# Kernel tuning notes

Hardware: AMD Instinct MI355X
Metric: run time of the kernel (lower is better)

The kernel has to match this reference:

```python
import jax, jax.numpy as jnp
import numpy as np

B, N, C, H, W = 32, 8, 256, 4, 4


def setup_inputs() -> dict:
    key = jax.random.key(0)
    k1, k2 = jax.random.split(key)
    pred = jax.random.normal(k1, (B, N, C, H, W), dtype=jnp.float32)
    gt = jax.random.normal(k2, (B, N, C, H, W), dtype=jnp.float32)
    return {"pred": pred, "gt": gt}


def reference(pred, gt):
    b, n, c, h, w = pred.shape
    M = b * n * h * w
    # (B,N,C,H,W) -> (B,N,H,W,C) -> (M, C)
    p = jnp.transpose(pred, (0, 1, 3, 4, 2)).reshape(M, c)
    # (B,N,C,H,W) -> (C,B,N,H,W) -> (C, M)
    g = jnp.transpose(gt, (2, 0, 1, 3, 4)).reshape(c, M)
    lossmat = p @ g  # (M, M) similarity matrix
    # CrossEntropy with target = arange(M): -mean(log_softmax diag)
    logp = jax.nn.log_softmax(lossmat, axis=1)
    loss = -jnp.mean(jnp.diagonal(logp))
    # accuracy (no grad in original)
    top1 = jnp.argmax(lossmat, axis=1)
    acc = jnp.mean((top1 == jnp.arange(M)).astype(jnp.float32)) * 100.0
    return (loss, acc)
```

## Files before the change

kernel.cpp:

```cpp
#include <hip/hip_runtime.h>
#include <cstdint>

typedef __bf16 bf16x8 __attribute__((ext_vector_type(8)));
typedef float floatx4 __attribute__((ext_vector_type(4)));


#define OFF_X     (0u)
#define OFF_Y     (2u*1024*1024)
#define OFF_PMAX  (4u*1024*1024)
#define OFF_PSUM  (5u*1024*1024)
#define OFF_DIAG  (6u*1024*1024)
#define OFF_LPART (OFF_DIAG + 16384u)
#define OFF_CPART (OFF_LPART + 256u)
#define OFF_CNT   (OFF_CPART + 256u)

#define AS1C(p) ((const __attribute__((address_space(1))) void*)(const void*)(p))
#define AS3(p)  ((__attribute__((address_space(3))) void*)(void*)(p))

__global__ __launch_bounds__(256) void transpose_stage(
    const float* __restrict__ pred, const float* __restrict__ gt,
    unsigned short* __restrict__ Xs, unsigned short* __restrict__ Ys,
    int* __restrict__ cnt) {
  int blk = blockIdx.x;
  const int t = threadIdx.x;
  if (blk == 0 && t < 33) cnt[t] = 0;
  const float* src;
  unsigned short* dst;
  int slab;
  if (blk < 256) { src = pred; dst = Xs; slab = blk; }
  else           { src = gt;   dst = Ys; slab = blk - 256; }
  const float* sb = src + slab * 4096;
  const int rb = slab >> 3, rowhi = slab & 7;
  #pragma unroll
  for (int half = 0; half < 2; ++half) {
    int c_ = half * 256 + t;
    int rowlo = c_ & 15;
    int quad  = (c_ >> 4) & 3;
    int kk    = (c_ >> 6) & 1;
    int s     = c_ >> 7;
    int k0 = s * 64 + kk * 32 + quad * 8;
    unsigned int packed[4];
    #pragma unroll
    for (int jj = 0; jj < 4; ++jj) {
      unsigned int lohi[2];
      #pragma unroll
      for (int e = 0; e < 2; ++e) {
        float f = sb[(k0 + jj * 2 + e) * 16 + rowlo];
        unsigned int u = __float_as_uint(f);
        lohi[e] = (u + 0x7FFFu + ((u >> 16) & 1u)) >> 16;
      }
      packed[jj] = lohi[0] | (lohi[1] << 16);
    }
    unsigned short* o = dst + rb * 32768 +
        (unsigned)(s * 1024 + kk * 512 + rowhi * 64 + quad * 16 + rowlo) * 8;
    uint4 v; v.x = packed[0]; v.y = packed[1]; v.z = packed[2]; v.w = packed[3];
    *reinterpret_cast<uint4*>(o) = v;
  }
}

__global__ __launch_bounds__(512) void gemm_softmax_partial(
    const unsigned short* __restrict__ Xs, const unsigned short* __restrict__ Ys,
    float* __restrict__ pmax, float* __restrict__ psum, float* __restrict__ diag) {
  __shared__ __align__(16) unsigned short As[2][16384];
  __shared__ __align__(16) unsigned short Bs[2][16384];
  const int t = threadIdx.x;
  const int wave = t >> 6, lane = t & 63;
  const int rg = wave >> 2, cg = wave & 3;
  const int bC = blockIdx.x, bR = blockIdx.y;
  const unsigned short* Ag = Xs + bR * 65536;
  const unsigned short* Bg = Ys + bC * 65536;

  floatx4 acc[8][4];
  const floatx4 zero = {0.f, 0.f, 0.f, 0.f};
  #pragma unroll
  for (int i = 0; i < 8; ++i)
    #pragma unroll
    for (int j = 0; j < 4; ++j) acc[i][j] = zero;

  auto STAGE = [&](int buf, int s) {
    #pragma unroll
    for (int it = 0; it < 4; ++it) {
      int chunk = it * 512 + t;
      int half = chunk >> 10, w_ = chunk & 1023;
      __builtin_amdgcn_global_load_lds(
          AS1C(Ag + half * 32768 + s * 8192 + w_ * 8),
          AS3(&As[buf][(unsigned)chunk * 8]), 16, 0, 0);
      __builtin_amdgcn_global_load_lds(
          AS1C(Bg + half * 32768 + s * 8192 + w_ * 8),
          AS3(&Bs[buf][(unsigned)chunk * 8]), 16, 0, 0);
    }
  };

  STAGE(0, 0);
  __syncthreads();
  int buf = 0;
  for (int s = 0; s < 4; ++s) {
    if (s < 3) STAGE(buf ^ 1, s + 1);
    #pragma unroll
    for (int kk = 0; kk < 2; ++kk) {
      bf16x8 b[4];
      #pragma unroll
      for (int fc = 0; fc < 4; ++fc) {
        int gc = cg * 4 + fc;
        b[fc] = *reinterpret_cast<const bf16x8*>(
            &Bs[buf][(unsigned)((gc >> 3) * 8192 + kk * 4096 +
                                (gc & 7) * 512 + lane * 8)]);
      }
      #pragma unroll
      for (int fr = 0; fr < 8; ++fr) {
        bf16x8 a = *reinterpret_cast<const bf16x8*>(
            &As[buf][(unsigned)(rg * 8192 + kk * 4096 + fr * 512 + lane * 8)]);
        #pragma unroll
        for (int fc = 0; fc < 4; ++fc)
          acc[fr][fc] = __builtin_amdgcn_mfma_f32_16x16x32_bf16(
              a, b[fc], acc[fr][fc], 0, 0, 0);
      }
    }
    if (s < 3) { __syncthreads(); buf ^= 1; }
  }

  const int quad = lane >> 4, lc = lane & 15;

  if (bR == bC) {
    #pragma unroll
    for (int fr = 0; fr < 8; ++fr) {
      if (cg == 2 * rg + (fr >> 2)) {
        #pragma unroll
        for (int r = 0; r < 4; ++r)
          if (lc == quad * 4 + r)
            diag[bR * 256 + rg * 128 + fr * 16 + lc] = acc[fr][fr & 3][r];
      }
    }
  }

  #pragma unroll
  for (int fr = 0; fr < 8; ++fr) {
    #pragma unroll
    for (int r = 0; r < 4; ++r) {
      float v0 = acc[fr][0][r], v1 = acc[fr][1][r];
      float v2 = acc[fr][2][r], v3 = acc[fr][3][r];
      float m = fmaxf(fmaxf(v0, v1), fmaxf(v2, v3));
      #pragma unroll
      for (int sh = 1; sh < 16; sh <<= 1) m = fmaxf(m, __shfl_xor(m, sh, 64));
      float ss = __expf(v0 - m) + __expf(v1 - m) +
                 __expf(v2 - m) + __expf(v3 - m);
      #pragma unroll
      for (int sh = 1; sh < 16; sh <<= 1) ss += __shfl_xor(ss, sh, 64);
      if (lc == 0) {
        int grow = bR * 256 + rg * 128 + fr * 16 + quad * 4 + r;
        int p = grow * 64 + bC * 4 + cg;
        pmax[p] = m; psum[p] = ss;
      }
    }
  }
}

__global__ __launch_bounds__(256) void combine_rows(
    const float* __restrict__ pmax, const float* __restrict__ psum,
    const float* __restrict__ diag,
    float* __restrict__ lpart, float* __restrict__ cpart,
    int* __restrict__ cnt, float* __restrict__ out) {
  int row = blockIdx.x * 256 + threadIdx.x;
  const float* pm = pmax + row * 64;
  const float* ps = psum + row * 64;
  float M = -3.4e38f;
  #pragma unroll 8
  for (int b = 0; b < 64; ++b) M = fmaxf(M, pm[b]);
  float S = 0.f;
  #pragma unroll 8
  for (int b = 0; b < 64; ++b) S += ps[b] * __expf(pm[b] - M);
  float d = diag[row];
  float lossr = logf(S) + M - d;
  float corr = (d == M) ? 1.f : 0.f;
  #pragma unroll
  for (int sh = 1; sh < 64; sh <<= 1) {
    lossr += __shfl_xor(lossr, sh, 64);
    corr  += __shfl_xor(corr,  sh, 64);
  }
  __shared__ float ls[4], cs[4];
  int wave = threadIdx.x >> 6, lane = threadIdx.x & 63;
  if (lane == 0) { ls[wave] = lossr; cs[wave] = corr; }
  __syncthreads();
  if (threadIdx.x == 0) {
    lpart[blockIdx.x] = ls[0] + ls[1] + ls[2] + ls[3];
    cpart[blockIdx.x] = cs[0] + cs[1] + cs[2] + cs[3];
    __threadfence();
    if (atomicAdd(cnt, 1) == 15) {
      __threadfence();
      float L = 0.f, C = 0.f;
      for (int i = 0; i < 16; ++i) { L += lpart[i]; C += cpart[i]; }
      out[0] = L * (1.f / 4096.f);
      out[1] = C * (100.f / 4096.f);
    }
  }
}

extern "C" void kernel_launch(void* const* d_in, const int* in_sizes, int n_in,
                              void* d_out, int out_size, void* d_ws, size_t ws_size,
                              hipStream_t stream) {
  const float* pred = (const float*)d_in[0];
  const float* gt   = (const float*)d_in[1];
  char* w = (char*)d_ws;
  unsigned short* Xbf = (unsigned short*)(w + OFF_X);
  unsigned short* Ybf = (unsigned short*)(w + OFF_Y);
  float* pmax  = (float*)(w + OFF_PMAX);
  float* psum  = (float*)(w + OFF_PSUM);
  float* diag  = (float*)(w + OFF_DIAG);
  float* lpart = (float*)(w + OFF_LPART);
  float* cpart = (float*)(w + OFF_CPART);
  int*   cnt   = (int*)(w + OFF_CNT);
  float* out   = (float*)d_out;

  transpose_stage<<<512, 256, 0, stream>>>(pred, gt, Xbf, Ybf, cnt);
  dim3 g1(16, 16);
  gemm_softmax_partial<<<g1, 512, 0, stream>>>(Xbf, Ybf, pmax, psum, diag);
  combine_rows<<<16, 256, 0, stream>>>(pmax, psum, diag, lpart, cpart, cnt, out);
}
```

Baseline: 94.06 us.

## Fuse fp32-to-bf16 transpose into GEMM staging with swizzled LDS layout

Removes the separate transpose/convert kernel and makes the GEMM load fp32 pred/gt directly from global memory, convert to bf16 in registers and write to LDS. The LDS layout gets an XOR swizzle to avoid bank conflicts on the register-staged writes and reads. Loads for the next stage are software-pipelined through registers, replacing the async global_load_lds path. The cost is that each block re-reads and re-converts its fp32 input (16x redundancy across the grid), and register pressure rises.

```diff
diff --git a/kernel.cpp b/kernel.cpp
--- a/kernel.cpp
+++ b/kernel.cpp
@@ -5,8 +5,6 @@
 typedef float floatx4 __attribute__((ext_vector_type(4)));
 
 
-#define OFF_X     (0u)
-#define OFF_Y     (2u*1024*1024)
 #define OFF_PMAX  (4u*1024*1024)
 #define OFF_PSUM  (5u*1024*1024)
 #define OFF_DIAG  (6u*1024*1024)
@@ -14,61 +12,34 @@
 #define OFF_CPART (OFF_LPART + 256u)
 #define OFF_CNT   (OFF_CPART + 256u)
 
-#define AS1C(p) ((const __attribute__((address_space(1))) void*)(const void*)(p))
-#define AS3(p)  ((__attribute__((address_space(3))) void*)(void*)(p))
-
-__global__ __launch_bounds__(256) void transpose_stage(
+__device__ __forceinline__ unsigned rne16(float f) {
+  unsigned u = __float_as_uint(f);
+  return (u + 0x7FFFu + ((u >> 16) & 1u)) >> 16;
+}
+
+__global__ __launch_bounds__(512) void gemm_fused(
     const float* __restrict__ pred, const float* __restrict__ gt,
-    unsigned short* __restrict__ Xs, unsigned short* __restrict__ Ys,
-    int* __restrict__ cnt) {
-  int blk = blockIdx.x;
-  const int t = threadIdx.x;
-  if (blk == 0 && t < 33) cnt[t] = 0;
-  const float* src;
-  unsigned short* dst;
-  int slab;
-  if (blk < 256) { src = pred; dst = Xs; slab = blk; }
-  else           { src = gt;   dst = Ys; slab = blk - 256; }
-  const float* sb = src + slab * 4096;
-  const int rb = slab >> 3, rowhi = slab & 7;
-  #pragma unroll
-  for (int half = 0; half < 2; ++half) {
-    int c_ = half * 256 + t;
-    int rowlo = c_ & 15;
-    int quad  = (c_ >> 4) & 3;
-    int kk    = (c_ >> 6) & 1;
-    int s     = c_ >> 7;
-    int k0 = s * 64 + kk * 32 + quad * 8;
-    unsigned int packed[4];
-    #pragma unroll
-    for (int jj = 0; jj < 4; ++jj) {
-      unsigned int lohi[2];
-      #pragma unroll
-      for (int e = 0; e < 2; ++e) {
-        float f = sb[(k0 + jj * 2 + e) * 16 + rowlo];
-        unsigned int u = __float_as_uint(f);
-        lohi[e] = (u + 0x7FFFu + ((u >> 16) & 1u)) >> 16;
-      }
-      packed[jj] = lohi[0] | (lohi[1] << 16);
-    }
-    unsigned short* o = dst + rb * 32768 +
-        (unsigned)(s * 1024 + kk * 512 + rowhi * 64 + quad * 16 + rowlo) * 8;
-    uint4 v; v.x = packed[0]; v.y = packed[1]; v.z = packed[2]; v.w = packed[3];
-    *reinterpret_cast<uint4*>(o) = v;
-  }
-}
-
-__global__ __launch_bounds__(512) void gemm_softmax_partial(
-    const unsigned short* __restrict__ Xs, const unsigned short* __restrict__ Ys,
-    float* __restrict__ pmax, float* __restrict__ psum, float* __restrict__ diag) {
+    float* __restrict__ pmax, float* __restrict__ psum,
+    float* __restrict__ diag, int* __restrict__ cnt) {
   __shared__ __align__(16) unsigned short As[2][16384];
   __shared__ __align__(16) unsigned short Bs[2][16384];
   const int t = threadIdx.x;
   const int wave = t >> 6, lane = t & 63;
   const int rg = wave >> 2, cg = wave & 3;
   const int bC = blockIdx.x, bR = blockIdx.y;
-  const unsigned short* Ag = Xs + bR * 65536;
-  const unsigned short* Bg = Ys + bC * 65536;
+  if (bC == 0 && bR == 0 && t == 0) cnt[0] = 0;
+
+  const int sl = t >> 5;
+  const int kq8 = (t >> 2) & 7;
+  const int rq = t & 3;
+  const int quad_w = kq8 & 3;
+  const unsigned wbase = (unsigned)(((sl >> 3) << 13) + ((kq8 >> 2) << 12) +
+                                    ((sl & 7) << 9) + (quad_w << 7));
+  const float* pX = pred + (((bR << 4) + sl) << 12) + (kq8 << 7) + (rq << 2);
+  const float* pY = gt   + (((bC << 4) + sl) << 12) + (kq8 << 7) + (rq << 2);
+
+  const unsigned lxor = (unsigned)(((lane >> 4) << 7) +
+                                   (((lane & 15) ^ (lane >> 4)) << 3));
 
   floatx4 acc[8][4];
   const floatx4 zero = {0.f, 0.f, 0.f, 0.f};
@@ -77,47 +48,72 @@
     #pragma unroll
     for (int j = 0; j < 4; ++j) acc[i][j] = zero;
 
-  auto STAGE = [&](int buf, int s) {
-    #pragma unroll
-    for (int it = 0; it < 4; ++it) {
-      int chunk = it * 512 + t;
-      int half = chunk >> 10, w_ = chunk & 1023;
-      __builtin_amdgcn_global_load_lds(
-          AS1C(Ag + half * 32768 + s * 8192 + w_ * 8),
-          AS3(&As[buf][(unsigned)chunk * 8]), 16, 0, 0);
-      __builtin_amdgcn_global_load_lds(
-          AS1C(Bg + half * 32768 + s * 8192 + w_ * 8),
-          AS3(&Bs[buf][(unsigned)chunk * 8]), 16, 0, 0);
-    }
-  };
-
-  STAGE(0, 0);
+  float4 xa[8], ya[8];
+
+#define LOADS(S) do {                                                        \
+    _Pragma("unroll") for (int j = 0; j < 8; ++j)                            \
+      xa[j] = *reinterpret_cast<const float4*>(pX + ((S) << 10) + (j << 4)); \
+    _Pragma("unroll") for (int j = 0; j < 8; ++j)                            \
+      ya[j] = *reinterpret_cast<const float4*>(pY + ((S) << 10) + (j << 4)); \
+  } while (0)
+
+#define STG_ROW(BUF, RR, COMP) do {                                          \
+    uint4 v;                                                                 \
+    unsigned off = wbase + (unsigned)((((rq << 2) + (RR)) ^ quad_w) << 3);   \
+    v.x = rne16(xa[0].COMP) | (rne16(xa[1].COMP) << 16);                     \
+    v.y = rne16(xa[2].COMP) | (rne16(xa[3].COMP) << 16);                     \
+    v.z = rne16(xa[4].COMP) | (rne16(xa[5].COMP) << 16);                     \
+    v.w = rne16(xa[6].COMP) | (rne16(xa[7].COMP) << 16);                     \
+    *reinterpret_cast<uint4*>(&As[BUF][off]) = v;                            \
+    v.x = rne16(ya[0].COMP) | (rne16(ya[1].COMP) << 16);                     \
+    v.y = rne16(ya[2].COMP) | (rne16(ya[3].COMP) << 16);                     \
+    v.z = rne16(ya[4].COMP) | (rne16(ya[5].COMP) << 16);                     \
+    v.w = rne16(ya[6].COMP) | (rne16(ya[7].COMP) << 16);                     \
+    *reinterpret_cast<uint4*>(&Bs[BUF][off]) = v;                            \
+  } while (0)
+
+#define WRITES(BUF) do {                                                     \
+    STG_ROW(BUF, 0, x); STG_ROW(BUF, 1, y);                                  \
+    STG_ROW(BUF, 2, z); STG_ROW(BUF, 3, w);                                  \
+  } while (0)
+
+#define COMPUTE(BUF) do {                                                    \
+    _Pragma("unroll") for (int kk = 0; kk < 2; ++kk) {                       \
+      bf16x8 b[4];                                                           \
+      _Pragma("unroll") for (int fc = 0; fc < 4; ++fc) {                     \
+        int gc = cg * 4 + fc;                                                \
+        b[fc] = *reinterpret_cast<const bf16x8*>(                            \
+            &Bs[BUF][(unsigned)((gc >> 3) * 8192 + kk * 4096 +               \
+                                (gc & 7) * 512) + lxor]);                    \
+      }                                                                      \
+      _Pragma("unroll") for (int fr = 0; fr < 8; ++fr) {                     \
+        bf16x8 a = *reinterpret_cast<const bf16x8*>(                         \
+            &As[BUF][(unsigned)(rg * 8192 + kk * 4096 + fr * 512) + lxor]);  \
+        _Pragma("unroll") for (int fc = 0; fc < 4; ++fc)                     \
+          acc[fr][fc] = __builtin_amdgcn_mfma_f32_16x16x32_bf16(             \
+              a, b[fc], acc[fr][fc], 0, 0, 0);                               \
+      }                                                                      \
+    }                                                                        \
+  } while (0)
+
+  LOADS(0);
+  WRITES(0);
+  LOADS(1);
   __syncthreads();
+
   int buf = 0;
-  for (int s = 0; s < 4; ++s) {
-    if (s < 3) STAGE(buf ^ 1, s + 1);
-    #pragma unroll
-    for (int kk = 0; kk < 2; ++kk) {
-      bf16x8 b[4];
-      #pragma unroll
-      for (int fc = 0; fc < 4; ++fc) {
-        int gc = cg * 4 + fc;
-        b[fc] = *reinterpret_cast<const bf16x8*>(
-            &Bs[buf][(unsigned)((gc >> 3) * 8192 + kk * 4096 +
-                                (gc & 7) * 512 + lane * 8)]);
-      }
-      #pragma unroll
-      for (int fr = 0; fr < 8; ++fr) {
-        bf16x8 a = *reinterpret_cast<const bf16x8*>(
-            &As[buf][(unsigned)(rg * 8192 + kk * 4096 + fr * 512 + lane * 8)]);
-        #pragma unroll
-        for (int fc = 0; fc < 4; ++fc)
-          acc[fr][fc] = __builtin_amdgcn_mfma_f32_16x16x32_bf16(
-              a, b[fc], acc[fr][fc], 0, 0, 0);
-      }
-    }
-    if (s < 3) { __syncthreads(); buf ^= 1; }
-  }
+  COMPUTE(0);
+  WRITES(1); LOADS(2); __syncthreads(); buf = 1;
+  COMPUTE(1);
+  WRITES(0); LOADS(3); __syncthreads(); buf = 0;
+  COMPUTE(0);
+  WRITES(1); __syncthreads();
+  COMPUTE(1);
+
+#undef LOADS
+#undef STG_ROW
+#undef WRITES
+#undef COMPUTE
 
   const int quad = lane >> 4, lc = lane & 15;
 
@@ -201,8 +197,6 @@
   const float* pred = (const float*)d_in[0];
   const float* gt   = (const float*)d_in[1];
   char* w = (char*)d_ws;
-  unsigned short* Xbf = (unsigned short*)(w + OFF_X);
-  unsigned short* Ybf = (unsigned short*)(w + OFF_Y);
   float* pmax  = (float*)(w + OFF_PMAX);
   float* psum  = (float*)(w + OFF_PSUM);
   float* diag  = (float*)(w + OFF_DIAG);
@@ -211,8 +205,7 @@
   int*   cnt   = (int*)(w + OFF_CNT);
   float* out   = (float*)d_out;
 
-  transpose_stage<<<512, 256, 0, stream>>>(pred, gt, Xbf, Ybf, cnt);
   dim3 g1(16, 16);
-  gemm_softmax_partial<<<g1, 512, 0, stream>>>(Xbf, Ybf, pmax, psum, diag);
+  gemm_fused<<<g1, 512, 0, stream>>>(pred, gt, pmax, psum, diag, cnt);
   combine_rows<<<16, 256, 0, stream>>>(pmax, psum, diag, lpart, cpart, cnt, out);
 }
```

Result: no change. 92.98 us (-1.2%).

## Remap GEMM blocks per XCD and unroll K loop with explicit vmcnt barriers

Applied to the files above, without the earlier changes.

Blocks now use a 1D grid, and each block index is remapped so the blocks on one XCD share a small set of row and column tiles. This is meant to improve L2 reuse of the bf16 operand slabs. The 4-step K loop is fully unrolled with two tiles of global_load_lds kept in flight. Raw s_waitcnt vmcnt plus s_barrier replace __syncthreads, so the loads overlap the MFMA work more deeply. Correctness now depends on the hand-counted vmcnt values and on the assumption that blocks are dispatched round-robin across XCDs.

```diff
diff --git a/kernel.cpp b/kernel.cpp
--- a/kernel.cpp
+++ b/kernel.cpp
@@ -66,7 +66,10 @@
   const int t = threadIdx.x;
   const int wave = t >> 6, lane = t & 63;
   const int rg = wave >> 2, cg = wave & 3;
-  const int bC = blockIdx.x, bR = blockIdx.y;
+  const int h = blockIdx.x;
+  const int xcd = h & 7, slot = h >> 3;
+  const int bR = ((xcd >> 1) << 2) | (slot & 3);
+  const int bC = ((xcd & 1) << 3) | (slot >> 2);
   const unsigned short* Ag = Xs + bR * 65536;
   const unsigned short* Bg = Ys + bC * 65536;
 
@@ -77,47 +80,68 @@
     #pragma unroll
     for (int j = 0; j < 4; ++j) acc[i][j] = zero;
 
-  auto STAGE = [&](int buf, int s) {
-    #pragma unroll
-    for (int it = 0; it < 4; ++it) {
-      int chunk = it * 512 + t;
-      int half = chunk >> 10, w_ = chunk & 1023;
-      __builtin_amdgcn_global_load_lds(
-          AS1C(Ag + half * 32768 + s * 8192 + w_ * 8),
-          AS3(&As[buf][(unsigned)chunk * 8]), 16, 0, 0);
-      __builtin_amdgcn_global_load_lds(
-          AS1C(Bg + half * 32768 + s * 8192 + w_ * 8),
-          AS3(&Bs[buf][(unsigned)chunk * 8]), 16, 0, 0);
-    }
-  };
+#define STAGE(BUF, S) do {                                                   \
+    _Pragma("unroll") for (int it = 0; it < 4; ++it) {                       \
+      int chunk = it * 512 + t;                                 \
+      int half = chunk >> 10, w_ = chunk & 1023;                             \
+      __builtin_amdgcn_global_load_lds(                                      \
+          AS1C(Ag + half * 32768 + (S) * 8192 + w_ * 8),                     \
+          AS3(&As[BUF][(unsigned)chunk * 8]), 16, 0, 0);                     \
+      __builtin_amdgcn_global_load_lds(                                      \
+          AS1C(Bg + half * 32768 + (S) * 8192 + w_ * 8),                     \
+          AS3(&Bs[BUF][(unsigned)chunk * 8]), 16, 0, 0);                     \
+    }                                                                        \
+  } while (0)
+
+#define COMPUTE(BUF) do {                                                    \
+    _Pragma("unroll") for (int kk = 0; kk < 2; ++kk) {                       \
+      bf16x8 b[4];                                                           \
+      _Pragma("unroll") for (int fc = 0; fc < 4; ++fc) {                     \
+        int gc = cg * 4 + fc;                                                \
+        b[fc] = *reinterpret_cast<const bf16x8*>(                            \
+            &Bs[BUF][(unsigned)((gc >> 3) * 8192 + kk * 4096 +               \
+                                (gc & 7) * 512 + lane * 8)]);                \
+      }                                                                      \
+      _Pragma("unroll") for (int fr = 0; fr < 8; ++fr) {                     \
+        bf16x8 a = *reinterpret_cast<const bf16x8*>(                         \
+            &As[BUF][(unsigned)(rg * 8192 + kk * 4096 + fr * 512 +           \
+                                lane * 8)]);                                 \
+        _Pragma("unroll") for (int fc = 0; fc < 4; ++fc)                     \
+          acc[fr][fc] = __builtin_amdgcn_mfma_f32_16x16x32_bf16(             \
+              a, b[fc], acc[fr][fc], 0, 0, 0);                               \
+      }                                                                      \
+    }                                                                        \
+  } while (0)
+
+#define BAR_ACQ(N) do {                                                      \
+    asm volatile("s_waitcnt vmcnt(" #N ")" ::: "memory");                    \
+    __builtin_amdgcn_s_barrier();                                            \
+    asm volatile("" ::: "memory");                                           \
+  } while (0)
+#define BAR_REL() do {                                                       \
+    asm volatile("" ::: "memory");                                           \
+    __builtin_amdgcn_s_barrier();                                            \
+  } while (0)
 
   STAGE(0, 0);
-  __syncthreads();
-  int buf = 0;
-  for (int s = 0; s < 4; ++s) {
-    if (s < 3) STAGE(buf ^ 1, s + 1);
-    #pragma unroll
-    for (int kk = 0; kk < 2; ++kk) {
-      bf16x8 b[4];
-      #pragma unroll
-      for (int fc = 0; fc < 4; ++fc) {
-        int gc = cg * 4 + fc;
-        b[fc] = *reinterpret_cast<const bf16x8*>(
-            &Bs[buf][(unsigned)((gc >> 3) * 8192 + kk * 4096 +
-                                (gc & 7) * 512 + lane * 8)]);
-      }
-      #pragma unroll
-      for (int fr = 0; fr < 8; ++fr) {
-        bf16x8 a = *reinterpret_cast<const bf16x8*>(
-            &As[buf][(unsigned)(rg * 8192 + kk * 4096 + fr * 512 + lane * 8)]);
-        #pragma unroll
-        for (int fc = 0; fc < 4; ++fc)
-          acc[fr][fc] = __builtin_amdgcn_mfma_f32_16x16x32_bf16(
-              a, b[fc], acc[fr][fc], 0, 0, 0);
-      }
-    }
-    if (s < 3) { __syncthreads(); buf ^= 1; }
-  }
+  STAGE(1, 1);
+  BAR_ACQ(8);
+  COMPUTE(0);
+  BAR_REL();
+  STAGE(0, 2);
+  BAR_ACQ(8);
+  COMPUTE(1);
+  BAR_REL();
+  STAGE(1, 3);
+  BAR_ACQ(8);
+  COMPUTE(0);
+  BAR_ACQ(0);
+  COMPUTE(1);
+
+#undef STAGE
+#undef COMPUTE
+#undef BAR_ACQ
+#undef BAR_REL
 
   const int quad = lane >> 4, lc = lane & 15;
 
@@ -212,7 +236,6 @@
   float* out   = (float*)d_out;
 
   transpose_stage<<<512, 256, 0, stream>>>(pred, gt, Xbf, Ybf, cnt);
-  dim3 g1(16, 16);
-  gemm_softmax_partial<<<g1, 512, 0, stream>>>(Xbf, Ybf, pmax, psum, diag);
+  gemm_softmax_partial<<<256, 512, 0, stream>>>(Xbf, Ybf, pmax, psum, diag);
   combine_rows<<<16, 256, 0, stream>>>(pmax, psum, diag, lpart, cpart, cnt, out);
 }
```

Result: no change. 94.20 us (+0.1%).

## Replace LDS-staged GEMM with direct-register per-wave tiles and XCD-aware block mapping

Applied to the files above, without the earlier changes.

The GEMM kernel no longer stages A and B tiles through double-buffered shared memory with barriers. Each wave now loads its bf16 fragments straight from global memory into registers and computes a 64x64 output tile. The grid grows from 256 blocks of 512 threads to 1024 blocks of 256 threads, and the block-to-tile mapping is arranged so blocks on the same XCD share rows and columns for L2 reuse. This removes LDS traffic and synchronisation and raises occupancy, at the cost of more redundant global/L2 loads because waves no longer share operands through LDS.

```diff
diff --git a/kernel.cpp b/kernel.cpp
--- a/kernel.cpp
+++ b/kernel.cpp
@@ -13,9 +13,6 @@
 #define OFF_LPART (OFF_DIAG + 16384u)
 #define OFF_CPART (OFF_LPART + 256u)
 #define OFF_CNT   (OFF_CPART + 256u)
-
-#define AS1C(p) ((const __attribute__((address_space(1))) void*)(const void*)(p))
-#define AS3(p)  ((__attribute__((address_space(3))) void*)(void*)(p))
 
 __global__ __launch_bounds__(256) void transpose_stage(
     const float* __restrict__ pred, const float* __restrict__ gt,
@@ -58,83 +55,60 @@
   }
 }
 
-__global__ __launch_bounds__(512) void gemm_softmax_partial(
+__global__ __launch_bounds__(256, 4) void gemm_wave(
     const unsigned short* __restrict__ Xs, const unsigned short* __restrict__ Ys,
     float* __restrict__ pmax, float* __restrict__ psum, float* __restrict__ diag) {
-  __shared__ __align__(16) unsigned short As[2][16384];
-  __shared__ __align__(16) unsigned short Bs[2][16384];
   const int t = threadIdx.x;
-  const int wave = t >> 6, lane = t & 63;
-  const int rg = wave >> 2, cg = wave & 3;
-  const int bC = blockIdx.x, bR = blockIdx.y;
-  const unsigned short* Ag = Xs + bR * 65536;
-  const unsigned short* Bg = Ys + bC * 65536;
+  const int wv = t >> 6, lane = t & 63;
+  const int b = blockIdx.x;
+  const int xcd = b & 7, slot = b >> 3;
+  const int rowb = ((xcd >> 1) << 4) | (slot & 15);
+  const int colb = ((xcd & 1) << 3) | (slot >> 4);
+  const int hh = rowb & 1, ch = wv & 1;
+  const unsigned short* Ab = Xs + (rowb >> 1) * 32768 + (unsigned)lane * 8;
+  const unsigned short* Bb = Ys + ((colb << 1) | (wv >> 1)) * 32768 +
+                             (unsigned)lane * 8;
 
-  floatx4 acc[8][4];
+  floatx4 acc[4][4];
   const floatx4 zero = {0.f, 0.f, 0.f, 0.f};
   #pragma unroll
-  for (int i = 0; i < 8; ++i)
+  for (int i = 0; i < 4; ++i)
     #pragma unroll
     for (int j = 0; j < 4; ++j) acc[i][j] = zero;
 
-  auto STAGE = [&](int buf, int s) {
+  #pragma unroll
+  for (int ks = 0; ks < 8; ++ks) {
+    const unsigned off = (unsigned)(((ks >> 1) * 1024 + (ks & 1) * 512)) * 8;
+    bf16x8 a[4], bf[4];
     #pragma unroll
-    for (int it = 0; it < 4; ++it) {
-      int chunk = it * 512 + t;
-      int half = chunk >> 10, w_ = chunk & 1023;
-      __builtin_amdgcn_global_load_lds(
-          AS1C(Ag + half * 32768 + s * 8192 + w_ * 8),
-          AS3(&As[buf][(unsigned)chunk * 8]), 16, 0, 0);
-      __builtin_amdgcn_global_load_lds(
-          AS1C(Bg + half * 32768 + s * 8192 + w_ * 8),
-          AS3(&Bs[buf][(unsigned)chunk * 8]), 16, 0, 0);
-    }
-  };
-
-  STAGE(0, 0);
-  __syncthreads();
-  int buf = 0;
-  for (int s = 0; s < 4; ++s) {
-    if (s < 3) STAGE(buf ^ 1, s + 1);
+    for (int fr = 0; fr < 4; ++fr)
+      a[fr] = *reinterpret_cast<const bf16x8*>(
+          Ab + off + (unsigned)((hh * 4 + fr) * 64) * 8);
     #pragma unroll
-    for (int kk = 0; kk < 2; ++kk) {
-      bf16x8 b[4];
+    for (int fc = 0; fc < 4; ++fc)
+      bf[fc] = *reinterpret_cast<const bf16x8*>(
+          Bb + off + (unsigned)((ch * 4 + fc) * 64) * 8);
+    #pragma unroll
+    for (int fr = 0; fr < 4; ++fr)
       #pragma unroll
-      for (int fc = 0; fc < 4; ++fc) {
-        int gc = cg * 4 + fc;
-        b[fc] = *reinterpret_cast<const bf16x8*>(
-            &Bs[buf][(unsigned)((gc >> 3) * 8192 + kk * 4096 +
-                                (gc & 7) * 512 + lane * 8)]);
-      }
-      #pragma unroll
-      for (int fr = 0; fr < 8; ++fr) {
-        bf16x8 a = *reinterpret_cast<const bf16x8*>(
-            &As[buf][(unsigned)(rg * 8192 + kk * 4096 + fr * 512 + lane * 8)]);
-        #pragma unroll
-        for (int fc = 0; fc < 4; ++fc)
-          acc[fr][fc] = __builtin_amdgcn_mfma_f32_16x16x32_bf16(
-              a, b[fc], acc[fr][fc], 0, 0, 0);
-      }
-    }
-    if (s < 3) { __syncthreads(); buf ^= 1; }
+      for (int fc = 0; fc < 4; ++fc)
+        acc[fr][fc] = __builtin_amdgcn_mfma_f32_16x16x32_bf16(
+            a[fr], bf[fc], acc[fr][fc], 0, 0, 0);
   }
 
   const int quad = lane >> 4, lc = lane & 15;
 
-  if (bR == bC) {
+  if (colb * 4 + wv == rowb) {
     #pragma unroll
-    for (int fr = 0; fr < 8; ++fr) {
-      if (cg == 2 * rg + (fr >> 2)) {
-        #pragma unroll
-        for (int r = 0; r < 4; ++r)
-          if (lc == quad * 4 + r)
-            diag[bR * 256 + rg * 128 + fr * 16 + lc] = acc[fr][fr & 3][r];
-      }
-    }
+    for (int fr = 0; fr < 4; ++fr)
+      #pragma unroll
+      for (int r = 0; r < 4; ++r)
+        if (lc == quad * 4 + r)
+          diag[rowb * 64 + fr * 16 + lc] = acc[fr][fr][r];
   }
 
   #pragma unroll
-  for (int fr = 0; fr < 8; ++fr) {
+  for (int fr = 0; fr < 4; ++fr) {
     #pragma unroll
     for (int r = 0; r < 4; ++r) {
       float v0 = acc[fr][0][r], v1 = acc[fr][1][r];
@@ -147,8 +121,8 @@
       #pragma unroll
       for (int sh = 1; sh < 16; sh <<= 1) ss += __shfl_xor(ss, sh, 64);
       if (lc == 0) {
-        int grow = bR * 256 + rg * 128 + fr * 16 + quad * 4 + r;
-        int p = grow * 64 + bC * 4 + cg;
+        int grow = rowb * 64 + fr * 16 + quad * 4 + r;
+        int p = grow * 64 + colb * 4 + wv;
         pmax[p] = m; psum[p] = ss;
       }
     }
@@ -212,7 +186,6 @@
   float* out   = (float*)d_out;
 
   transpose_stage<<<512, 256, 0, stream>>>(pred, gt, Xbf, Ybf, cnt);
-  dim3 g1(16, 16);
-  gemm_softmax_partial<<<g1, 512, 0, stream>>>(Xbf, Ybf, pmax, psum, diag);
+  gemm_wave<<<1024, 256, 0, stream>>>(Xbf, Ybf, pmax, psum, diag);
   combine_rows<<<16, 256, 0, stream>>>(pmax, psum, diag, lpart, cpart, cnt, out);
 }
```

Result: faster. 91.40 us (-2.8%).
